# Performance work log

Hardware: AMD Instinct MI355X
Metric: run time of the kernel (lower is better)

The kernel has to match this reference:

```python
import jax, jax.numpy as jnp
import numpy as np

N_NODES = 100000
N_EDGES = 1600000
HIDDEN = 256
CONV_OUT = 128
OUT = 2


def setup_inputs() -> dict:
    key = jax.random.key(0)
    k1, k2, k3, k4, k5, k6, k7 = jax.random.split(key, 7)
    x = jax.random.normal(k1, (N_NODES, HIDDEN), dtype=jnp.float32)
    edge_index = jax.random.randint(k2, (2, N_EDGES), 0, N_NODES, dtype=jnp.int64)
    edge_weight = jax.random.uniform(k3, (N_EDGES,), dtype=jnp.float32)
    # GCNConv parameters (lin: hidden->128, bias added after aggregation)
    W1 = jax.random.normal(k4, (HIDDEN, CONV_OUT), dtype=jnp.float32) / np.sqrt(HIDDEN)
    b1 = jnp.zeros((CONV_OUT,), dtype=jnp.float32)
    # head Linear(128, out_channels)
    W2 = jax.random.normal(k5, (CONV_OUT, OUT), dtype=jnp.float32) / np.sqrt(CONV_OUT)
    b2 = jax.random.normal(k6, (OUT,), dtype=jnp.float32) * 0.01
    return {"x": x, "edge_index": edge_index, "edge_weight": edge_weight,
            "W1": W1, "b1": b1, "W2": W2, "b2": b2}


def reference(x, edge_index, edge_weight, W1, b1, W2, b2):
    # GCNConv (use_weights=True branch, no relu), dropout in eval mode (identity), then Linear.
    N = x.shape[0]
    src, dst = edge_index[0], edge_index[1]
    # add self-loops with weight 1 (PyG default fill_value=1.0)
    loop = jnp.arange(N, dtype=src.dtype)
    src = jnp.concatenate([src, loop])
    dst = jnp.concatenate([dst, loop])
    w = jnp.concatenate([edge_weight, jnp.ones((N,), dtype=edge_weight.dtype)])
    # symmetric normalization: norm = d^{-1/2}[src] * w * d^{-1/2}[dst]
    deg = jax.ops.segment_sum(w, dst, num_segments=N)
    dinv = jnp.where(deg > 0, jax.lax.rsqrt(deg), 0.0)
    norm = dinv[src] * w * dinv[dst]
    # transform then gather-scatter aggregate
    h = x @ W1                                   # [N, 128]
    msgs = norm[:, None] * h[src]                # [E+N, 128]
    agg = jax.ops.segment_sum(msgs, dst, num_segments=N) + b1  # [N, 128]
    return agg @ W2 + b2                         # [N, out_channels]
```

## Files before the change

kernel.cpp:

```cpp
#include <hip/hip_runtime.h>

#define N_NODES 100000
#define N_EDGES 1600000
#define HIDDEN 256

#define BSH 7
#define BNODES 128
#define NB 782
#define NPB 256
#define EPB 6250
#define SLOTS 32
#define NZB 3125


__global__ __launch_bounds__(1024) void k_place(
        const int* __restrict__ ei, const float* __restrict__ ew,
        const float* __restrict__ W1, const float* __restrict__ b1,
        const float* __restrict__ W2, const float* __restrict__ b2,
        int* __restrict__ cnt, uint2* __restrict__ rec,
        float* __restrict__ W12, float* __restrict__ cvec) {
    const int tid = threadIdx.x, bid = blockIdx.x;
    if (bid == NPB) {
        if (tid < HIDDEN) {
            const float4* w1r = (const float4*)(W1 + (size_t)tid * 128);
            float a0 = 0.f, a1 = 0.f;
#pragma unroll 8
            for (int k4 = 0; k4 < 32; ++k4) {
                float4 v = w1r[k4];
                a0 += v.x * W2[8 * k4 + 0]; a1 += v.x * W2[8 * k4 + 1];
                a0 += v.y * W2[8 * k4 + 2]; a1 += v.y * W2[8 * k4 + 3];
                a0 += v.z * W2[8 * k4 + 4]; a1 += v.z * W2[8 * k4 + 5];
                a0 += v.w * W2[8 * k4 + 6]; a1 += v.w * W2[8 * k4 + 7];
            }
            W12[tid] = a0;
            W12[HIDDEN + tid] = a1;
            if (tid < 2) {
                float acc = b2[tid];
                for (int k = 0; k < 128; ++k) acc += b1[k] * W2[2 * k + tid];
                cvec[tid] = acc;
            }
        }
        return;
    }
    __shared__ int cursor[NB];
    for (int i = tid; i < NB; i += 1024) cursor[i] = 0;
    __syncthreads();
    const int e0 = bid * EPB, e1 = e0 + EPB;
    for (int e = e0 + tid; e < e1; e += 1024) {
        int d = ei[N_EDGES + e];
        int s = ei[e];
        float wv = ew[e];
        int bk = ((unsigned)d) >> BSH;
        int pos = atomicAdd(&cursor[bk], 1);
        if (pos < SLOTS)
            rec[((size_t)bk * NPB + bid) * SLOTS + pos] =
                make_uint2((unsigned)s | ((unsigned)(d & (BNODES - 1)) << 17),
                           __float_as_uint(wv));
    }
    __syncthreads();
    for (int i = tid; i < NB; i += 1024)
        cnt[(size_t)i * NPB + bid] = min(cursor[i], SLOTS);
}

__global__ __launch_bounds__(256) void k_zdeg(
        const float* __restrict__ x, const float* __restrict__ W12,
        const uint2* __restrict__ rec, const int* __restrict__ cnt,
        float* __restrict__ z, float* __restrict__ dinv) {
    __shared__ float tile[4][8][HIDDEN];
    __shared__ float acc[BNODES];
    const int tid = threadIdx.x, bid = blockIdx.x;
    if (bid < NZB) {
        const int wv   = tid >> 6;
        const int lane = tid & 63;
        const int sub  = lane & 7;
        const int nl   = lane >> 3;
        float4 wa[8], wb[8];
#pragma unroll
        for (int j = 0; j < 8; ++j) {
            wa[j] = *(const float4*)(W12 + (sub + 8 * j) * 4);
            wb[j] = *(const float4*)(W12 + HIDDEN + (sub + 8 * j) * 4);
        }
        const int rowbase = bid * 32 + wv * 8;
#pragma unroll
        for (int j = 0; j < 8; ++j) {
            const float* gsrc = x + (size_t)(rowbase + j) * HIDDEN + lane * 4;
            __builtin_amdgcn_global_load_lds(
                (const __attribute__((address_space(1))) void*)gsrc,
                (__attribute__((address_space(3))) void*)&tile[wv][j][0],
                16, 0, 0);
        }
        asm volatile("s_waitcnt vmcnt(0)" ::: "memory");
        float a0 = 0.f, a1 = 0.f;
#pragma unroll
        for (int j = 0; j < 8; ++j) {
            float4 v = *(const float4*)&tile[wv][nl][(sub + 8 * j) * 4];
            a0 += v.x * wa[j].x + v.y * wa[j].y + v.z * wa[j].z + v.w * wa[j].w;
            a1 += v.x * wb[j].x + v.y * wb[j].y + v.z * wb[j].z + v.w * wb[j].w;
        }
#pragma unroll
        for (int m = 1; m <= 4; m <<= 1) {
            a0 += __shfl_xor(a0, m, 64);
            a1 += __shfl_xor(a1, m, 64);
        }
        if (sub == 0) ((float2*)z)[rowbase + nl] = make_float2(a0, a1);
    } else {
        const int b = bid - NZB;
        if (tid < BNODES) acc[tid] = 1.0f;
        __syncthreads();
        const int n = cnt[(size_t)b * NPB + tid];
        const uint2* r = rec + ((size_t)b * NPB + tid) * SLOTS;
        int i = 0;
        for (; i + 2 <= n; i += 2) {
            uint4 q = *(const uint4*)(r + i);
            atomicAdd(&acc[q.x >> 17], __uint_as_float(q.y));
            atomicAdd(&acc[q.z >> 17], __uint_as_float(q.w));
        }
        if (i < n) {
            uint2 q = r[i];
            atomicAdd(&acc[q.x >> 17], __uint_as_float(q.y));
        }
        __syncthreads();
        if (tid < BNODES) {
            int node = b * BNODES + tid;
            if (node < N_NODES) dinv[node] = rsqrtf(acc[tid]);
        }
    }
}

__global__ __launch_bounds__(256) void k_gather(
        const uint2* __restrict__ rec, const int* __restrict__ cnt,
        const float* __restrict__ dinv, const float* __restrict__ z,
        const float* __restrict__ cvec, float2* __restrict__ out) {
    __shared__ float ax[BNODES], ay[BNODES];
    const int tid = threadIdx.x, b = blockIdx.x;
    if (tid < BNODES) { ax[tid] = 0.f; ay[tid] = 0.f; }
    __syncthreads();
    const int n = cnt[(size_t)b * NPB + tid];
    const uint2* r = rec + ((size_t)b * NPB + tid) * SLOTS;
    int i = 0;
    for (; i + 2 <= n; i += 2) {
        uint4 q = *(const uint4*)(r + i);
        int s0 = (int)(q.x & 0x1FFFFu), s1 = (int)(q.z & 0x1FFFFu);
        float di0 = dinv[s0], di1 = dinv[s1];
        float2 z0 = ((const float2*)z)[s0];
        float2 z1 = ((const float2*)z)[s1];
        float nw0 = di0 * __uint_as_float(q.y);
        float nw1 = di1 * __uint_as_float(q.w);
        int d0 = (int)(q.x >> 17), d1 = (int)(q.z >> 17);
        atomicAdd(&ax[d0], nw0 * z0.x);
        atomicAdd(&ay[d0], nw0 * z0.y);
        atomicAdd(&ax[d1], nw1 * z1.x);
        atomicAdd(&ay[d1], nw1 * z1.y);
    }
    if (i < n) {
        uint2 q = r[i];
        int s = (int)(q.x & 0x1FFFFu);
        float nw = dinv[s] * __uint_as_float(q.y);
        float2 zv = ((const float2*)z)[s];
        int dl = (int)(q.x >> 17);
        atomicAdd(&ax[dl], nw * zv.x);
        atomicAdd(&ay[dl], nw * zv.y);
    }
    __syncthreads();
    if (tid < BNODES) {
        int node = b * BNODES + tid;
        if (node < N_NODES) {
            float di = dinv[node];
            float2 zv = ((const float2*)z)[node];
            out[node] = make_float2(di * ax[tid] + di * di * zv.x + cvec[0],
                                    di * ay[tid] + di * di * zv.y + cvec[1]);
        }
    }
}

extern "C" void kernel_launch(void* const* d_in, const int* in_sizes, int n_in,
                              void* d_out, int out_size, void* d_ws, size_t ws_size,
                              hipStream_t stream) {
    const float* x  = (const float*)d_in[0];
    const int*   ei = (const int*)d_in[1];
    const float* ew = (const float*)d_in[2];
    const float* W1 = (const float*)d_in[3];
    const float* b1 = (const float*)d_in[4];
    const float* W2 = (const float*)d_in[5];
    const float* b2 = (const float*)d_in[6];
    float2* out = (float2*)d_out;

    char* ws = (char*)d_ws;
    uint2*  rec  = (uint2*)ws;           size_t off = (size_t)NB * NPB * SLOTS * 8;
    int*    cnt  = (int*)(ws + off);     off += (size_t)NB * NPB * 4;
    float*  dinv = (float*)(ws + off);   off += (size_t)N_NODES * 4;
    float*  z    = (float*)(ws + off);   off += (size_t)N_NODES * 8;
    float*  W12  = (float*)(ws + off);   off += HIDDEN * 2 * 4;
    float*  cvec = (float*)(ws + off);   off += 16;

    k_place <<<NPB + 1, 1024, 0, stream>>>(ei, ew, W1, b1, W2, b2, cnt, rec, W12, cvec);
    k_zdeg  <<<NZB + NB, 256, 0, stream>>>(x, W12, rec, cnt, z, dinv);
    k_gather<<<NB, 256, 0, stream>>>(rec, cnt, dinv, z, cvec, out);
}
```

Measured before the change: 78.82 us.

## Double-buffer x tiles per wave with multiple chunks per wave in z projection

Each wave of the z-projection part of k_zdeg now handles several 4-row chunks and double-buffers them in LDS, issuing the async global-to-LDS load for the next chunk before computing the current one. Block count falls to about half, and the LDS rows are padded to reduce bank conflicts. The goal is to overlap the HBM streaming of x with compute and cut per-block launch overhead. In exchange there is less block-level parallelism and a partial vmcnt wait that must be correct.

```diff
diff --git a/kernel.cpp b/kernel.cpp
--- a/kernel.cpp
+++ b/kernel.cpp
@@ -10,7 +10,10 @@
 #define NPB 256
 #define EPB 6250
 #define SLOTS 32
-#define NZB 3125
+#define NCH 25000
+#define CPW 4
+#define NZB 1563
+#define RPAD 260
 
 
 __global__ __launch_bounds__(1024) void k_place(
@@ -66,43 +69,64 @@
         const float* __restrict__ x, const float* __restrict__ W12,
         const uint2* __restrict__ rec, const int* __restrict__ cnt,
         float* __restrict__ z, float* __restrict__ dinv) {
-    __shared__ float tile[4][8][HIDDEN];
+    __shared__ float tile[4][2][4][RPAD];
     __shared__ float acc[BNODES];
     const int tid = threadIdx.x, bid = blockIdx.x;
     if (bid < NZB) {
         const int wv   = tid >> 6;
         const int lane = tid & 63;
-        const int sub  = lane & 7;
-        const int nl   = lane >> 3;
-        float4 wa[8], wb[8];
-#pragma unroll
-        for (int j = 0; j < 8; ++j) {
-            wa[j] = *(const float4*)(W12 + (sub + 8 * j) * 4);
-            wb[j] = *(const float4*)(W12 + HIDDEN + (sub + 8 * j) * 4);
-        }
-        const int rowbase = bid * 32 + wv * 8;
-#pragma unroll
-        for (int j = 0; j < 8; ++j) {
-            const float* gsrc = x + (size_t)(rowbase + j) * HIDDEN + lane * 4;
-            __builtin_amdgcn_global_load_lds(
-                (const __attribute__((address_space(1))) void*)gsrc,
-                (__attribute__((address_space(3))) void*)&tile[wv][j][0],
-                16, 0, 0);
-        }
-        asm volatile("s_waitcnt vmcnt(0)" ::: "memory");
-        float a0 = 0.f, a1 = 0.f;
-#pragma unroll
-        for (int j = 0; j < 8; ++j) {
-            float4 v = *(const float4*)&tile[wv][nl][(sub + 8 * j) * 4];
-            a0 += v.x * wa[j].x + v.y * wa[j].y + v.z * wa[j].z + v.w * wa[j].w;
-            a1 += v.x * wb[j].x + v.y * wb[j].y + v.z * wb[j].z + v.w * wb[j].w;
-        }
-#pragma unroll
-        for (int m = 1; m <= 4; m <<= 1) {
-            a0 += __shfl_xor(a0, m, 64);
-            a1 += __shfl_xor(a1, m, 64);
-        }
-        if (sub == 0) ((float2*)z)[rowbase + nl] = make_float2(a0, a1);
+        const int sub  = lane & 15;
+        const int nl   = lane >> 4;
+        float4 wa[4], wb[4];
+#pragma unroll
+        for (int j = 0; j < 4; ++j) {
+            wa[j] = *(const float4*)(W12 + (sub + 16 * j) * 4);
+            wb[j] = *(const float4*)(W12 + HIDDEN + (sub + 16 * j) * 4);
+        }
+        const int c0   = (bid * 4 + wv) * CPW;
+        const int cend = (c0 + CPW < NCH) ? c0 + CPW : NCH;
+        if (c0 < cend) {
+#pragma unroll
+            for (int j = 0; j < 4; ++j) {
+                const float* gsrc = x + (size_t)(c0 * 4 + j) * HIDDEN + lane * 4;
+                __builtin_amdgcn_global_load_lds(
+                    (const __attribute__((address_space(1))) void*)gsrc,
+                    (__attribute__((address_space(3))) void*)&tile[wv][0][j][0],
+                    16, 0, 0);
+            }
+            int buf = 0;
+            for (int c = c0; c < cend; ++c) {
+                const bool more = (c + 1 < cend);
+                if (more) {
+#pragma unroll
+                    for (int j = 0; j < 4; ++j) {
+                        const float* gsrc = x + (size_t)((c + 1) * 4 + j) * HIDDEN + lane * 4;
+                        __builtin_amdgcn_global_load_lds(
+                            (const __attribute__((address_space(1))) void*)gsrc,
+                            (__attribute__((address_space(3))) void*)&tile[wv][buf ^ 1][j][0],
+                            16, 0, 0);
+                    }
+                    asm volatile("s_waitcnt vmcnt(4)" ::: "memory");
+                } else {
+                    asm volatile("s_waitcnt vmcnt(0)" ::: "memory");
+                }
+                __builtin_amdgcn_sched_barrier(0);
+                float a0 = 0.f, a1 = 0.f;
+#pragma unroll
+                for (int j = 0; j < 4; ++j) {
+                    const float4 v = *(const float4*)&tile[wv][buf][nl][(sub + 16 * j) * 4];
+                    a0 += v.x * wa[j].x + v.y * wa[j].y + v.z * wa[j].z + v.w * wa[j].w;
+                    a1 += v.x * wb[j].x + v.y * wb[j].y + v.z * wb[j].z + v.w * wb[j].w;
+                }
+#pragma unroll
+                for (int m = 1; m <= 8; m <<= 1) {
+                    a0 += __shfl_xor(a0, m, 64);
+                    a1 += __shfl_xor(a1, m, 64);
+                }
+                if (sub == 0) ((float2*)z)[c * 4 + nl] = make_float2(a0, a1);
+                buf ^= 1;
+            }
+        }
     } else {
         const int b = bid - NZB;
         if (tid < BNODES) acc[tid] = 1.0f;
```

Measured after the change: 79.80 us. Within noise of the previous version (+1.3%).
